# Kernel tuning notes

Hardware: AMD Instinct MI355X
Metric: run time of the kernel (lower is better)

The kernel has to match this reference:

```python
import jax, jax.numpy as jnp
import numpy as np

N = 100000        # nodes
E = 3200000       # edges (avg degree 32)
B = 64            # graphs in the batch
IN_DIM = 128
HEADS = 4
C1 = 8            # conv1 out_channels per head
C2 = 4            # conv2 out_channels per head
OUT_DIM = 10
EPS = 1e-16       # PyG softmax denominator eps


def _lin(key, fan_in, fan_out):
    return jax.random.normal(key, (fan_in, fan_out), jnp.float32) / np.sqrt(fan_in)


def setup_inputs() -> dict:
    key = jax.random.key(0)
    ks = jax.random.split(key, 16)
    x = jax.random.normal(ks[0], (N, IN_DIM), jnp.float32)
    edge_index = jax.random.randint(ks[1], (2, E), 0, N)
    batch = jnp.sort(jax.random.randint(ks[2], (N,), 0, B))
    d1 = HEADS * C1  # 32
    d2 = HEADS * C2  # 16
    inp = {
        "x": x, "edge_index": edge_index, "batch": batch,
        # conv1 (TransformerConv in=128 -> heads*8 = 32)
        "Wq1": _lin(ks[3], IN_DIM, d1), "bq1": jnp.zeros((d1,), jnp.float32),
        "Wk1": _lin(ks[4], IN_DIM, d1), "bk1": jnp.zeros((d1,), jnp.float32),
        "Wv1": _lin(ks[5], IN_DIM, d1), "bv1": jnp.zeros((d1,), jnp.float32),
        "Ws1": _lin(ks[6], IN_DIM, d1), "bs1": jnp.zeros((d1,), jnp.float32),
        # conv2 (in=32 -> heads*4 = 16)
        "Wq2": _lin(ks[7], d1, d2), "bq2": jnp.zeros((d2,), jnp.float32),
        "Wk2": _lin(ks[8], d1, d2), "bk2": jnp.zeros((d2,), jnp.float32),
        "Wv2": _lin(ks[9], d1, d2), "bv2": jnp.zeros((d2,), jnp.float32),
        "Ws2": _lin(ks[10], d1, d2), "bs2": jnp.zeros((d2,), jnp.float32),
        # fc (16 -> 10)
        "Wfc": _lin(ks[11], d2, OUT_DIM), "bfc": jnp.zeros((OUT_DIM,), jnp.float32),
    }
    return inp


def transformer_conv(x, src, dst, Wq, bq, Wk, bk, Wv, bv, Ws, bs, heads):
    n = x.shape[0]
    hc = Wq.shape[1]
    c = hc // heads
    q = (x @ Wq + bq).reshape(n, heads, c)
    k = (x @ Wk + bk).reshape(n, heads, c)
    v = (x @ Wv + bv).reshape(n, heads, c)
    # edge-wise attention logits: query at dst, key at src -> [E, H]
    alpha = jnp.einsum('ehc,ehc->eh', q[dst], k[src]) / np.sqrt(c).astype(np.float32)
    # segment softmax over incoming edges of each dst node
    amax = jax.ops.segment_max(alpha, dst, num_segments=n)           # [N,H]
    ea = jnp.exp(alpha - amax[dst])
    denom = jax.ops.segment_sum(ea, dst, num_segments=n)             # [N,H]
    w = ea / (denom[dst] + EPS)                                      # [E,H]
    msg = v[src] * w[:, :, None]                                     # [E,H,C]
    out = jax.ops.segment_sum(msg, dst, num_segments=n).reshape(n, hc)
    return out + x @ Ws + bs  # root/skip connection


def reference(x, edge_index, batch,
              Wq1, bq1, Wk1, bk1, Wv1, bv1, Ws1, bs1,
              Wq2, bq2, Wk2, bk2, Wv2, bv2, Ws2, bs2,
              Wfc, bfc):
    src, dst = edge_index[0], edge_index[1]
    h = transformer_conv(x, src, dst, Wq1, bq1, Wk1, bk1, Wv1, bv1, Ws1, bs1, HEADS)
    h = jax.nn.relu(h)
    h = transformer_conv(h, src, dst, Wq2, bq2, Wk2, bk2, Wv2, bv2, Ws2, bs2, HEADS)
    h = jax.nn.relu(h)
    # global mean pool per graph
    sums = jax.ops.segment_sum(h, batch, num_segments=B)             # [B,16]
    cnt = jax.ops.segment_sum(jnp.ones((h.shape[0],), h.dtype), batch, num_segments=B)
    pooled = sums / jnp.maximum(cnt, 1.0)[:, None]
    return pooled @ Wfc + bfc                                        # [B,OUT_DIM]
```

## Files before the change

### kernel.cpp

```cpp
#include <hip/hip_runtime.h>

#define HEADS 4
#define EPS 1e-16f
#define NR 256
#define EPB 2048

typedef float floatx2 __attribute__((ext_vector_type(2)));
typedef short bf16x8 __attribute__((ext_vector_type(8)));
typedef float f32x4 __attribute__((ext_vector_type(4)));

__device__ inline unsigned short f2bf(float f) {
    union { float f; unsigned u; } v; v.f = f;
    unsigned r = v.u + 0x7FFFu + ((v.u >> 16) & 1u);
    return (unsigned short)(r >> 16);
}
__device__ inline unsigned char f2fp8(float f) {
    return (unsigned char)(__builtin_amdgcn_cvt_pk_fp8_f32(f, 0.f, 0u, false) & 0xFF);
}

__device__ inline int rangeOf(int dst, int rdiv, float rinv) {
    int q = (int)((float)dst * rinv);
    if (q > NR - 1) q = NR - 1;
    if ((long long)q * rdiv > dst) --q;
    else if ((long long)(q + 1) * rdiv <= dst) ++q;
    return q;
}

__global__ __launch_bounds__(256) void scatter_count(
    const int* __restrict__ ei, int E, int rdiv, float rinv,
    int* __restrict__ pcnt)
{
    __shared__ int cnt[NR];
    int b = blockIdx.x, t = threadIdx.x;
    int b0 = b * EPB;
    int nloc = min(EPB, E - b0);
    cnt[t] = 0;
    __syncthreads();
    #pragma unroll
    for (int u = 0; u < 8; ++u) {
        int li = u * 256 + t;
        if (li < nloc)
            atomicAdd(&cnt[rangeOf(ei[E + b0 + li], rdiv, rinv)], 1);
    }
    __syncthreads();
    pcnt[(size_t)b * NR + t] = cnt[t];
}

__global__ __launch_bounds__(256) void qprefix(
    int* __restrict__ pcnt, int nb, int* __restrict__ qtot)
{
    __shared__ int part[256];
    int q = blockIdx.x, t = threadIdx.x;
    int per = (nb + 255) >> 8;
    int lo = t * per, hi = min(lo + per, nb);
    int s = 0;
    for (int b = lo; b < hi; ++b) s += pcnt[(size_t)b * NR + q];
    part[t] = s;
    __syncthreads();
    for (int off = 1; off < 256; off <<= 1) {
        int a = (t >= off) ? part[t - off] : 0;
        __syncthreads();
        part[t] += a;
        __syncthreads();
    }
    if (t == 255) qtot[q] = part[255];
    int pre = (t == 0) ? 0 : part[t - 1];
    for (int b = lo; b < hi; ++b) {
        int c = pcnt[(size_t)b * NR + q];
        pcnt[(size_t)b * NR + q] = pre;
        pre += c;
    }
}

__global__ void qscan(const int* __restrict__ qtot, int* __restrict__ rstart)
{
    __shared__ int tmp[NR];
    int t = threadIdx.x;
    tmp[t] = qtot[t];
    __syncthreads();
    for (int off = 1; off < NR; off <<= 1) {
        int a = (t >= off) ? tmp[t - off] : 0;
        __syncthreads();
        tmp[t] += a;
        __syncthreads();
    }
    rstart[t] = (t == 0) ? 0 : tmp[t - 1];
    if (t == NR - 1) rstart[NR] = tmp[NR - 1];
}

__global__ __launch_bounds__(256) void scatter_place(
    const int* __restrict__ ei, int E, int rdiv, float rinv,
    const int* __restrict__ pcnt, const int* __restrict__ rstart,
    int* __restrict__ rsrc, int* __restrict__ rdst)
{
    __shared__ int2 lrec[EPB];
    __shared__ unsigned char lq[EPB];
    __shared__ int cnt[NR], base[NR], scn[NR];
    int b = blockIdx.x, t = threadIdx.x;
    int b0 = b * EPB;
    int nloc = min(EPB, E - b0);
    cnt[t] = 0;
    __syncthreads();
    int myq[8], myoff[8];
    int2 myrec[8];
    #pragma unroll
    for (int u = 0; u < 8; ++u) {
        int li = u * 256 + t;
        if (li < nloc) {
            int e = b0 + li;
            int sv = ei[e], dv = ei[E + e];
            int q = rangeOf(dv, rdiv, rinv);
            myq[u] = q;
            myrec[u] = make_int2(sv, dv);
            myoff[u] = atomicAdd(&cnt[q], 1);
        } else myq[u] = -1;
    }
    __syncthreads();
    scn[t] = cnt[t];
    __syncthreads();
    for (int off = 1; off < 256; off <<= 1) {
        int a = (t >= off) ? scn[t - off] : 0;
        __syncthreads();
        scn[t] += a;
        __syncthreads();
    }
    base[t] = (t == 0) ? 0 : scn[t - 1];
    __syncthreads();
    #pragma unroll
    for (int u = 0; u < 8; ++u) {
        if (myq[u] >= 0) {
            int slot = base[myq[u]] + myoff[u];
            lrec[slot] = myrec[u];
            lq[slot] = (unsigned char)myq[u];
        }
    }
    __syncthreads();
    #pragma unroll
    for (int u = 0; u < 8; ++u) {
        int s2 = u * 256 + t;
        if (s2 < nloc) {
            int q = lq[s2];
            int g = rstart[q] + pcnt[(size_t)b * NR + q] + (s2 - base[q]);
            int2 r = lrec[s2];
            rsrc[g] = r.x;
            rdst[g] = r.y;
        }
    }
}

__global__ __launch_bounds__(256) void deg_range_place(
    const int* __restrict__ rsrc, const int* __restrict__ rdst,
    const int* __restrict__ rstart,
    int* __restrict__ deg, int* __restrict__ row_ptr, int* __restrict__ phd,
    int* __restrict__ col, int n, int rdiv, int E)
{
    __shared__ int h[512];
    __shared__ int cur[512];
    __shared__ int psum[256];
    __shared__ int hd[256];
    int q = blockIdx.x, t = threadIdx.x;
    int lo = q * rdiv, hi = min(lo + rdiv, n);
    int nn = hi - lo;
    if (nn <= 0) {
        phd[q * 256 + t] = 0;
        if (t == 0 && q == NR - 1) row_ptr[n] = E;
        return;
    }
    h[t] = 0; h[t + 256] = 0; hd[t] = 0;
    __syncthreads();
    int rlo = rstart[q], rhi = rstart[q + 1];
    for (int i = rlo + t; i < rhi; i += 256)
        atomicAdd(&h[rdst[i] - lo], 1);
    __syncthreads();
    int s0 = h[2 * t], s1 = h[2 * t + 1];
    psum[t] = s0 + s1;
    __syncthreads();
    for (int off = 1; off < 256; off <<= 1) {
        int a = (t >= off) ? psum[t - off] : 0;
        __syncthreads();
        psum[t] += a;
        __syncthreads();
    }
    int base = rlo + ((t == 0) ? 0 : psum[t - 1]);
    cur[2 * t] = base;
    cur[2 * t + 1] = base + s0;
    if (2 * t < nn) {
        row_ptr[lo + 2 * t] = base;
        deg[lo + 2 * t] = s0;
        atomicAdd(&hd[min(s0, 255)], 1);
    }
    if (2 * t + 1 < nn) {
        row_ptr[lo + 2 * t + 1] = base + s0;
        deg[lo + 2 * t + 1] = s1;
        atomicAdd(&hd[min(s1, 255)], 1);
    }
    if (t == 0 && q == NR - 1) row_ptr[n] = E;
    __syncthreads();
    phd[q * 256 + t] = hd[t];
    for (int i = rlo + t; i < rhi; i += 256) {
        int pos = atomicAdd(&cur[rdst[i] - lo], 1);
        col[pos] = rsrc[i];
    }
}

__global__ __launch_bounds__(256) void dsort_scanA(
    int* __restrict__ phd, int* __restrict__ tot)
{
    __shared__ int tmp[256];
    int bin = blockIdx.x, t = threadIdx.x;
    int v = phd[t * 256 + bin];
    tmp[t] = v;
    __syncthreads();
    for (int off = 1; off < 256; off <<= 1) {
        int a = (t >= off) ? tmp[t - off] : 0;
        __syncthreads();
        tmp[t] += a;
        __syncthreads();
    }
    phd[t * 256 + bin] = tmp[t] - v;
    if (t == 255) tot[bin] = tmp[255];
}

__global__ void dsort_scanB(int* __restrict__ tot)
{
    __shared__ int tmp[256];
    int t = threadIdx.x;
    int v = tot[t];
    tmp[t] = v;
    __syncthreads();
    for (int off = 1; off < 256; off <<= 1) {
        int a = (t >= off) ? tmp[t - off] : 0;
        __syncthreads();
        tmp[t] += a;
        __syncthreads();
    }
    tot[t] = tmp[t] - v;
}

__global__ __launch_bounds__(256) void dsort_place(
    const int* __restrict__ phd, const int* __restrict__ tot,
    const int* __restrict__ deg, int* __restrict__ order, int n, int rdiv)
{
    __shared__ int lcur[256];
    int q = blockIdx.x, t = threadIdx.x;
    lcur[t] = phd[q * 256 + t] + tot[t];
    __syncthreads();
    int lo = q * rdiv, hi = min(lo + rdiv, n);
    for (int i = lo + t; i < hi; i += 256) {
        int pos = atomicAdd(&lcur[min(deg[i], 255)], 1);
        order[pos] = i;
    }
}

__global__ __launch_bounds__(256) void pack_w1(
    const float* __restrict__ Wq, const float* __restrict__ Wk,
    const float* __restrict__ Wv, const float* __restrict__ Ws,
    unsigned short* __restrict__ wp)
{
    int tid = blockIdx.x * 256 + threadIdx.x;
    int s = tid >> 9, c = (tid >> 6) & 7, l = tid & 63;
    int gcol = c * 16 + (l & 15);
    int sub = gcol >> 5, j = gcol & 31;
    const float* W = (sub == 0) ? Wq : (sub == 1) ? Wk : (sub == 2) ? Wv : Ws;
    int k0 = s * 32 + ((l >> 4) << 3);
    unsigned short v[8];
    #pragma unroll
    for (int jj = 0; jj < 8; ++jj) v[jj] = f2bf(W[(size_t)(k0 + jj) * 32 + j]);
    uint4 o;
    o.x = v[0] | ((unsigned)v[1] << 16);
    o.y = v[2] | ((unsigned)v[3] << 16);
    o.z = v[4] | ((unsigned)v[5] << 16);
    o.w = v[6] | ((unsigned)v[7] << 16);
    *(uint4*)(wp + (size_t)tid * 8) = o;
}

__global__ void pack_w2(
    const float* __restrict__ Wq, const float* __restrict__ Wk,
    const float* __restrict__ Wv, const float* __restrict__ Ws,
    unsigned short* __restrict__ wp)
{
    int tid = threadIdx.x;
    int c = tid >> 6, l = tid & 63;
    int gcol = c * 16 + (l & 15);
    int sub = gcol >> 4, j = gcol & 15;
    const float* W = (sub == 0) ? Wq : (sub == 1) ? Wk : (sub == 2) ? Wv : Ws;
    int k0 = (l >> 4) << 3;
    unsigned short v[8];
    #pragma unroll
    for (int jj = 0; jj < 8; ++jj) v[jj] = f2bf(W[(size_t)(k0 + jj) * 16 + j]);
    uint4 o;
    o.x = v[0] | ((unsigned)v[1] << 16);
    o.y = v[2] | ((unsigned)v[3] << 16);
    o.z = v[4] | ((unsigned)v[5] << 16);
    o.w = v[6] | ((unsigned)v[7] << 16);
    *(uint4*)(wp + (size_t)tid * 8) = o;
}

__global__ __launch_bounds__(256) void proj1_mfma(
    const float* __restrict__ x, const unsigned short* __restrict__ wp,
    const float* __restrict__ bq, const float* __restrict__ bk,
    const float* __restrict__ bv, const float* __restrict__ bs,
    float* __restrict__ qs1, unsigned char* __restrict__ kv1, int n)
{
    int w = threadIdx.x >> 6, l = threadIdx.x & 63;
    int row0 = blockIdx.x * 64 + w * 16;
    if (row0 >= n) return;
    int arow = row0 + (l & 15);
    f32x4 c0 = {0,0,0,0}, c1 = {0,0,0,0}, c2 = {0,0,0,0}, c3 = {0,0,0,0};
    f32x4 c4 = {0,0,0,0}, c5 = {0,0,0,0}, c6 = {0,0,0,0}, c7 = {0,0,0,0};
    const uint4* wp4 = (const uint4*)wp;
    #pragma unroll
    for (int s = 0; s < 4; ++s) {
        union { uint4 u; bf16x8 b; } av;
        if (arow < n) {
            const float* xp = x + (size_t)arow * 128 + s * 32 + ((l >> 4) << 3);
            float4 x0 = *(const float4*)xp;
            float4 x1 = *(const float4*)(xp + 4);
            av.u.x = f2bf(x0.x) | ((unsigned)f2bf(x0.y) << 16);
            av.u.y = f2bf(x0.z) | ((unsigned)f2bf(x0.w) << 16);
            av.u.z = f2bf(x1.x) | ((unsigned)f2bf(x1.y) << 16);
            av.u.w = f2bf(x1.z) | ((unsigned)f2bf(x1.w) << 16);
        } else {
            av.u = make_uint4(0, 0, 0, 0);
        }
        const uint4* base = wp4 + (size_t)(s * 8) * 64 + l;
        union { uint4 u; bf16x8 b; } bc;
        bc.u = base[0 * 64]; c0 = __builtin_amdgcn_mfma_f32_16x16x32_bf16(av.b, bc.b, c0, 0, 0, 0);
        bc.u = base[1 * 64]; c1 = __builtin_amdgcn_mfma_f32_16x16x32_bf16(av.b, bc.b, c1, 0, 0, 0);
        bc.u = base[2 * 64]; c2 = __builtin_amdgcn_mfma_f32_16x16x32_bf16(av.b, bc.b, c2, 0, 0, 0);
        bc.u = base[3 * 64]; c3 = __builtin_amdgcn_mfma_f32_16x16x32_bf16(av.b, bc.b, c3, 0, 0, 0);
        bc.u = base[4 * 64]; c4 = __builtin_amdgcn_mfma_f32_16x16x32_bf16(av.b, bc.b, c4, 0, 0, 0);
        bc.u = base[5 * 64]; c5 = __builtin_amdgcn_mfma_f32_16x16x32_bf16(av.b, bc.b, c5, 0, 0, 0);
        bc.u = base[6 * 64]; c6 = __builtin_amdgcn_mfma_f32_16x16x32_bf16(av.b, bc.b, c6, 0, 0, 0);
        bc.u = base[7 * 64]; c7 = __builtin_amdgcn_mfma_f32_16x16x32_bf16(av.b, bc.b, c7, 0, 0, 0);
    }
    int rbase = row0 + ((l >> 4) << 2);
    int lc = l & 15;
    int pkA = ((lc >> 3) << 4) + (lc & 7);
    int pkB = ((2 + (lc >> 3)) << 4) + (lc & 7);
    int pvA = pkA + 8;
    int pvB = pkB + 8;
    float bq0 = bq[lc], bq1 = bq[16 + lc];
    float bk0 = bk[lc], bk1 = bk[16 + lc];
    float bv0 = bv[lc], bv1 = bv[16 + lc];
    float bs0 = bs[lc], bs1 = bs[16 + lc];
    #pragma unroll
    for (int r = 0; r < 4; ++r) {
        int row = rbase + r;
        if (row < n) {
            float* q = qs1 + (size_t)row * 64;
            unsigned char* kvp = kv1 + (size_t)row * 64;
            q[lc]      = c0[r] + bq0;
            q[16 + lc] = c1[r] + bq1;
            q[32 + lc] = c6[r] + bs0;
            q[48 + lc] = c7[r] + bs1;
            kvp[pkA] = f2fp8(c2[r] + bk0);
            kvp[pkB] = f2fp8(c3[r] + bk1);
            kvp[pvA] = f2fp8(c4[r] + bv0);
            kvp[pvB] = f2fp8(c5[r] + bv1);
        }
    }
}

__global__ __launch_bounds__(256) void proj2_mfma(
    const float* __restrict__ h1, const unsigned short* __restrict__ wp,
    const float* __restrict__ bq, const float* __restrict__ bk,
    const float* __restrict__ bv, const float* __restrict__ bs,
    float* __restrict__ qs2, unsigned char* __restrict__ kv2, int n)
{
    int w = threadIdx.x >> 6, l = threadIdx.x & 63;
    int row0 = blockIdx.x * 64 + w * 16;
    if (row0 >= n) return;
    int arow = row0 + (l & 15);
    f32x4 c0 = {0,0,0,0}, c1 = {0,0,0,0}, c2 = {0,0,0,0}, c3 = {0,0,0,0};
    union { uint4 u; bf16x8 b; } av;
    if (arow < n) {
        const float* xp = h1 + (size_t)arow * 32 + ((l >> 4) << 3);
        float4 x0 = *(const float4*)xp;
        float4 x1 = *(const float4*)(xp + 4);
        av.u.x = f2bf(x0.x) | ((unsigned)f2bf(x0.y) << 16);
        av.u.y = f2bf(x0.z) | ((unsigned)f2bf(x0.w) << 16);
        av.u.z = f2bf(x1.x) | ((unsigned)f2bf(x1.y) << 16);
        av.u.w = f2bf(x1.z) | ((unsigned)f2bf(x1.w) << 16);
    } else {
        av.u = make_uint4(0, 0, 0, 0);
    }
    const uint4* base = (const uint4*)wp + l;
    union { uint4 u; bf16x8 b; } bc;
    bc.u = base[0];   c0 = __builtin_amdgcn_mfma_f32_16x16x32_bf16(av.b, bc.b, c0, 0, 0, 0);
    bc.u = base[64];  c1 = __builtin_amdgcn_mfma_f32_16x16x32_bf16(av.b, bc.b, c1, 0, 0, 0);
    bc.u = base[128]; c2 = __builtin_amdgcn_mfma_f32_16x16x32_bf16(av.b, bc.b, c2, 0, 0, 0);
    bc.u = base[192]; c3 = __builtin_amdgcn_mfma_f32_16x16x32_bf16(av.b, bc.b, c3, 0, 0, 0);
    int rbase = row0 + ((l >> 4) << 2);
    int lc = l & 15;
    int pk = ((lc >> 2) << 3) + (lc & 3);
    int pv = pk + 4;
    float bq0 = bq[lc], bk0 = bk[lc], bv0 = bv[lc], bs0 = bs[lc];
    #pragma unroll
    for (int r = 0; r < 4; ++r) {
        int row = rbase + r;
        if (row < n) {
            float* q = qs2 + (size_t)row * 32;
            unsigned char* kvp = kv2 + (size_t)row * 32;
            q[lc]      = c0[r] + bq0;
            q[16 + lc] = c3[r] + bs0;
            kvp[pk] = f2fp8(c1[r] + bk0);
            kvp[pv] = f2fp8(c2[r] + bv0);
        }
    }
}

__global__ __launch_bounds__(256) void gather_conv1(
    const int* __restrict__ row_ptr, const int* __restrict__ order,
    const int* __restrict__ col, const float* __restrict__ qs1,
    const unsigned char* __restrict__ kv1, float* __restrict__ h1, int n)
{
    int tid = blockIdx.x * 256 + threadIdx.x;
    if (tid >= n * HEADS) return;
    int node = order[tid >> 2], h = tid & 3;
    const float4* qp = (const float4*)(qs1 + (size_t)node * 64 + h * 8);
    float4 q0 = qp[0], q1 = qp[1];
    int start = row_ptr[node], d = row_ptr[node + 1] - start;
    float m = -INFINITY, s = 0.f;
    float a0x=0,a0y=0,a0z=0,a0w=0,a1x=0,a1y=0,a1z=0,a1w=0;
    if (d > 0) {
        int dm1 = d - 1;
        uint4 kv = *(const uint4*)(kv1 + (size_t)col[start] * 64 + h * 16);
        int c1 = col[start + min(1, dm1)];
        for (int i = 0; i < d; ++i) {
            int c2 = col[start + min(i + 2, dm1)];
            uint4 kvn = *(const uint4*)(kv1 + (size_t)c1 * 64 + h * 16);
            floatx2 k01 = __builtin_amdgcn_cvt_pk_f32_fp8(kv.x, false);
            floatx2 k23 = __builtin_amdgcn_cvt_pk_f32_fp8(kv.x, true);
            floatx2 k45 = __builtin_amdgcn_cvt_pk_f32_fp8(kv.y, false);
            floatx2 k67 = __builtin_amdgcn_cvt_pk_f32_fp8(kv.y, true);
            float a = (q0.x*k01.x + q0.y*k01.y + q0.z*k23.x + q0.w*k23.y
                     + q1.x*k45.x + q1.y*k45.y + q1.z*k67.x + q1.w*k67.y)
                    * 0.35355339059327373f;
            float mn = fmaxf(m, a);
            float corr = __expf(m - mn);
            float ea = __expf(a - mn);
            s = s * corr + ea;
            floatx2 v01 = __builtin_amdgcn_cvt_pk_f32_fp8(kv.z, false);
            floatx2 v23 = __builtin_amdgcn_cvt_pk_f32_fp8(kv.z, true);
            floatx2 v45 = __builtin_amdgcn_cvt_pk_f32_fp8(kv.w, false);
            floatx2 v67 = __builtin_amdgcn_cvt_pk_f32_fp8(kv.w, true);
            a0x = a0x*corr + ea*v01.x; a0y = a0y*corr + ea*v01.y;
            a0z = a0z*corr + ea*v23.x; a0w = a0w*corr + ea*v23.y;
            a1x = a1x*corr + ea*v45.x; a1y = a1y*corr + ea*v45.y;
            a1z = a1z*corr + ea*v67.x; a1w = a1w*corr + ea*v67.y;
            m = mn;
            kv = kvn; c1 = c2;
        }
    }
    float inv = 1.f / (s + EPS);
    const float* sk = qs1 + (size_t)node * 64 + 32 + h * 8;
    float4 o0, o1;
    o0.x = fmaxf(a0x*inv + sk[0], 0.f); o0.y = fmaxf(a0y*inv + sk[1], 0.f);
    o0.z = fmaxf(a0z*inv + sk[2], 0.f); o0.w = fmaxf(a0w*inv + sk[3], 0.f);
    o1.x = fmaxf(a1x*inv + sk[4], 0.f); o1.y = fmaxf(a1y*inv + sk[5], 0.f);
    o1.z = fmaxf(a1z*inv + sk[6], 0.f); o1.w = fmaxf(a1w*inv + sk[7], 0.f);
    float4* op = (float4*)(h1 + (size_t)node * 32 + h * 8);
    op[0] = o0; op[1] = o1;
}

__global__ __launch_bounds__(256) void gather_conv2(
    const int* __restrict__ row_ptr, const int* __restrict__ order,
    const int* __restrict__ col, const float* __restrict__ qs2,
    const unsigned char* __restrict__ kv2, float* __restrict__ h2, int n)
{
    int tid = blockIdx.x * 256 + threadIdx.x;
    if (tid >= n * HEADS) return;
    int node = order[tid >> 2], h = tid & 3;
    float4 q = *(const float4*)(qs2 + (size_t)node * 32 + h * 4);
    int start = row_ptr[node], d = row_ptr[node + 1] - start;
    float m = -INFINITY, s = 0.f;
    float ax=0, ay=0, az=0, aw=0;
    if (d > 0) {
        int dm1 = d - 1;
        uint2 kv = *(const uint2*)(kv2 + (size_t)col[start] * 32 + h * 8);
        int c1 = col[start + min(1, dm1)];
        for (int i = 0; i < d; ++i) {
            int c2 = col[start + min(i + 2, dm1)];
            uint2 kvn = *(const uint2*)(kv2 + (size_t)c1 * 32 + h * 8);
            floatx2 k01 = __builtin_amdgcn_cvt_pk_f32_fp8(kv.x, false);
            floatx2 k23 = __builtin_amdgcn_cvt_pk_f32_fp8(kv.x, true);
            float a = (q.x*k01.x + q.y*k01.y + q.z*k23.x + q.w*k23.y) * 0.5f;
            float mn = fmaxf(m, a);
            float corr = __expf(m - mn);
            float ea = __expf(a - mn);
            s = s * corr + ea;
            floatx2 v01 = __builtin_amdgcn_cvt_pk_f32_fp8(kv.y, false);
            floatx2 v23 = __builtin_amdgcn_cvt_pk_f32_fp8(kv.y, true);
            ax = ax*corr + ea*v01.x; ay = ay*corr + ea*v01.y;
            az = az*corr + ea*v23.x; aw = aw*corr + ea*v23.y;
            m = mn;
            kv = kvn; c1 = c2;
        }
    }
    float inv = 1.f / (s + EPS);
    const float* sk = qs2 + (size_t)node * 32 + 16 + h * 4;
    float4 o;
    o.x = fmaxf(ax*inv + sk[0], 0.f);
    o.y = fmaxf(ay*inv + sk[1], 0.f);
    o.z = fmaxf(az*inv + sk[2], 0.f);
    o.w = fmaxf(aw*inv + sk[3], 0.f);
    *(float4*)(h2 + (size_t)node * 16 + h * 4) = o;
}

__global__ __launch_bounds__(256) void pool_kernel(
    const float* __restrict__ h2, const int* __restrict__ batch,
    float* __restrict__ pooled, float* __restrict__ cnt, int n)
{
    __shared__ float acc[16];
    __shared__ int bShared;
    __shared__ int uniform;
    int node0 = blockIdx.x * 16;
    int t = threadIdx.x;
    int node = node0 + (t >> 4), j = t & 15;
    if (t == 0) {
        int bFirst = batch[node0];
        int bLast = batch[min(node0 + 15, n - 1)];
        bShared = bFirst;
        uniform = (bFirst == bLast);
    }
    if (t < 16) acc[t] = 0.f;
    __syncthreads();
    bool active = node < n;
    float val = active ? h2[(size_t)node * 16 + j] : 0.f;
    if (uniform) {
        if (active) atomicAdd(&acc[j], val);
        __syncthreads();
        int nlocal = min(16, n - node0);
        if (t < 16) atomicAdd(pooled + bShared * 16 + t, acc[t]);
        if (t == 0) atomicAdd(cnt + bShared, (float)nlocal);
    } else {
        if (active) {
            int b = batch[node];
            atomicAdd(pooled + b * 16 + j, val);
            if (j == 0) atomicAdd(cnt + b, 1.f);
        }
    }
}

__global__ void fc_kernel(
    const float* __restrict__ pooled, const float* __restrict__ cnt,
    const float* __restrict__ Wfc, const float* __restrict__ bfc,
    float* __restrict__ out)
{
    int t = threadIdx.x;
    if (t < 64 * 10) {
        int b = t / 10, o = t % 10;
        float c = fmaxf(cnt[b], 1.0f);
        float acc = bfc[o];
        #pragma unroll
        for (int k = 0; k < 16; ++k)
            acc += (pooled[b * 16 + k] / c) * Wfc[k * 10 + o];
        out[t] = acc;
    }
}

extern "C" void kernel_launch(void* const* d_in, const int* in_sizes, int n_in,
                              void* d_out, int out_size, void* d_ws, size_t ws_size,
                              hipStream_t stream) {
    const float* x     = (const float*)d_in[0];
    const int*   ei    = (const int*)d_in[1];
    const int*   batch = (const int*)d_in[2];
    const float* Wq1 = (const float*)d_in[3],  *bq1 = (const float*)d_in[4];
    const float* Wk1 = (const float*)d_in[5],  *bk1 = (const float*)d_in[6];
    const float* Wv1 = (const float*)d_in[7],  *bv1 = (const float*)d_in[8];
    const float* Ws1 = (const float*)d_in[9],  *bs1 = (const float*)d_in[10];
    const float* Wq2 = (const float*)d_in[11], *bq2 = (const float*)d_in[12];
    const float* Wk2 = (const float*)d_in[13], *bk2 = (const float*)d_in[14];
    const float* Wv2 = (const float*)d_in[15], *bv2 = (const float*)d_in[16];
    const float* Ws2 = (const float*)d_in[17], *bs2 = (const float*)d_in[18];
    const float* Wfc = (const float*)d_in[19], *bfc = (const float*)d_in[20];

    int N = in_sizes[0] / 128;
    int E = in_sizes[1] / 2;
    int rdiv = (N + NR - 1) / NR;
    float rinv = 1.0f / (float)rdiv;
    int NB = (E + EPB - 1) / EPB;

    float* ws = (float*)d_ws;
    float* qs1    = ws;
    float* h1     = qs1 + (size_t)N * 64;
    float* h2     = h1 + (size_t)N * 32;
    float* qs2    = h2 + (size_t)N * 16;
    float* pooled = qs2 + (size_t)N * 32;
    float* cnt    = pooled + 1024;
    unsigned char* kv1 = (unsigned char*)(cnt + 64);
    unsigned char* kv2 = kv1 + (size_t)N * 64;
    int* deg     = (int*)(kv2 + (size_t)N * 32);
    int* row_ptr = deg + N;
    int* rstart  = row_ptr + N + 1;
    int* qtot    = rstart + NR + 1;
    int* col     = qtot + NR;
    int* order   = col + E;
    int* pcnt    = order + N;
    int* phd     = pcnt + (size_t)NB * NR;
    unsigned short* wp1 = (unsigned short*)(phd + (size_t)NR * 256);
    unsigned short* wp2 = wp1 + 16384;
    int* rsrc = (int*)h1;
    int* rdst = (int*)h2;

    hipMemsetAsync(pooled, 0, (1024 + 64) * sizeof(float), stream);

    int ngrid = (N * HEADS + 255) / 256;
    int mtiles = (N + 63) / 64;

    pack_w1<<<8, 256, 0, stream>>>(Wq1, Wk1, Wv1, Ws1, wp1);
    pack_w2<<<1, 256, 0, stream>>>(Wq2, Wk2, Wv2, Ws2, wp2);

    scatter_count<<<NB, 256, 0, stream>>>(ei, E, rdiv, rinv, pcnt);
    qprefix<<<NR, 256, 0, stream>>>(pcnt, NB, qtot);
    qscan<<<1, NR, 0, stream>>>(qtot, rstart);
    scatter_place<<<NB, 256, 0, stream>>>(ei, E, rdiv, rinv, pcnt, rstart, rsrc, rdst);
    deg_range_place<<<NR, 256, 0, stream>>>(rsrc, rdst, rstart, deg, row_ptr, phd, col, N, rdiv, E);
    dsort_scanA<<<NR, 256, 0, stream>>>(phd, qtot);
    dsort_scanB<<<1, 256, 0, stream>>>(qtot);
    dsort_place<<<NR, 256, 0, stream>>>(phd, qtot, deg, order, N, rdiv);

    proj1_mfma<<<mtiles, 256, 0, stream>>>(x, wp1, bq1, bk1, bv1, bs1, qs1, kv1, N);
    gather_conv1<<<ngrid, 256, 0, stream>>>(row_ptr, order, col, qs1, kv1, h1, N);

    proj2_mfma<<<mtiles, 256, 0, stream>>>(h1, wp2, bq2, bk2, bv2, bs2, qs2, kv2, N);
    gather_conv2<<<ngrid, 256, 0, stream>>>(row_ptr, order, col, qs2, kv2, h2, N);

    pool_kernel<<<(N + 15) / 16, 256, 0, stream>>>(h2, batch, pooled, cnt, N);
    fc_kernel<<<1, 640, 0, stream>>>(pooled, cnt, Wfc, bfc, (float*)d_out);
}
```

Measured before the change: 312.1 us.

## Store K/V head-major and assign one head per gather block

Projection kernels now write fp8 K/V in a head-major layout ([head][node][16 or 8 bytes]) instead of node-major. The gather kernels map each block to a single head, so every thread gathers from a compact per-head array. This aims to shrink each head's working set and improve cache-line use per head. The cost is that the four heads of a node are no longer read by adjacent lanes, so row_ptr, col and q loads are repeated across blocks and a shared 64B line is split into separate accesses.

New measurement: 705.7 us. 2.26x slower.

```diff
diff --git a/kernel.cpp b/kernel.cpp
--- a/kernel.cpp
+++ b/kernel.cpp
@@ -336,10 +336,8 @@
     }
     int rbase = row0 + ((l >> 4) << 2);
     int lc = l & 15;
-    int pkA = ((lc >> 3) << 4) + (lc & 7);
-    int pkB = ((2 + (lc >> 3)) << 4) + (lc & 7);
-    int pvA = pkA + 8;
-    int pvB = pkB + 8;
+    int hA = lc >> 3, eA = lc & 7;
+    int hB = 2 + (lc >> 3);
     float bq0 = bq[lc], bq1 = bq[16 + lc];
     float bk0 = bk[lc], bk1 = bk[16 + lc];
     float bv0 = bv[lc], bv1 = bv[16 + lc];
@@ -349,15 +347,14 @@
         int row = rbase + r;
         if (row < n) {
             float* q = qs1 + (size_t)row * 64;
-            unsigned char* kvp = kv1 + (size_t)row * 64;
             q[lc]      = c0[r] + bq0;
             q[16 + lc] = c1[r] + bq1;
             q[32 + lc] = c6[r] + bs0;
             q[48 + lc] = c7[r] + bs1;
-            kvp[pkA] = f2fp8(c2[r] + bk0);
-            kvp[pkB] = f2fp8(c3[r] + bk1);
-            kvp[pvA] = f2fp8(c4[r] + bv0);
-            kvp[pvB] = f2fp8(c5[r] + bv1);
+            kv1[((size_t)hA * n + row) * 16 + eA]     = f2fp8(c2[r] + bk0);
+            kv1[((size_t)hB * n + row) * 16 + eA]     = f2fp8(c3[r] + bk1);
+            kv1[((size_t)hA * n + row) * 16 + 8 + eA] = f2fp8(c4[r] + bv0);
+            kv1[((size_t)hB * n + row) * 16 + 8 + eA] = f2fp8(c5[r] + bv1);
         }
     }
 }
@@ -393,19 +390,17 @@
     bc.u = base[192]; c3 = __builtin_amdgcn_mfma_f32_16x16x32_bf16(av.b, bc.b, c3, 0, 0, 0);
     int rbase = row0 + ((l >> 4) << 2);
     int lc = l & 15;
-    int pk = ((lc >> 2) << 3) + (lc & 3);
-    int pv = pk + 4;
+    int hh = lc >> 2, ee = lc & 3;
     float bq0 = bq[lc], bk0 = bk[lc], bv0 = bv[lc], bs0 = bs[lc];
     #pragma unroll
     for (int r = 0; r < 4; ++r) {
         int row = rbase + r;
         if (row < n) {
             float* q = qs2 + (size_t)row * 32;
-            unsigned char* kvp = kv2 + (size_t)row * 32;
             q[lc]      = c0[r] + bq0;
             q[16 + lc] = c3[r] + bs0;
-            kvp[pk] = f2fp8(c1[r] + bk0);
-            kvp[pv] = f2fp8(c2[r] + bv0);
+            kv2[((size_t)hh * n + row) * 8 + ee]     = f2fp8(c1[r] + bk0);
+            kv2[((size_t)hh * n + row) * 8 + 4 + ee] = f2fp8(c2[r] + bv0);
         }
     }
 }
@@ -415,9 +410,11 @@
     const int* __restrict__ col, const float* __restrict__ qs1,
     const unsigned char* __restrict__ kv1, float* __restrict__ h1, int n)
 {
-    int tid = blockIdx.x * 256 + threadIdx.x;
-    if (tid >= n * HEADS) return;
-    int node = order[tid >> 2], h = tid & 3;
+    int h = blockIdx.x & 3;
+    int idx = (blockIdx.x >> 2) * 256 + threadIdx.x;
+    if (idx >= n) return;
+    int node = order[idx];
+    const unsigned char* kvh = kv1 + (size_t)h * n * 16;
     const float4* qp = (const float4*)(qs1 + (size_t)node * 64 + h * 8);
     float4 q0 = qp[0], q1 = qp[1];
     int start = row_ptr[node], d = row_ptr[node + 1] - start;
@@ -425,11 +422,11 @@
     float a0x=0,a0y=0,a0z=0,a0w=0,a1x=0,a1y=0,a1z=0,a1w=0;
     if (d > 0) {
         int dm1 = d - 1;
-        uint4 kv = *(const uint4*)(kv1 + (size_t)col[start] * 64 + h * 16);
+        uint4 kv = *(const uint4*)(kvh + (size_t)col[start] * 16);
         int c1 = col[start + min(1, dm1)];
         for (int i = 0; i < d; ++i) {
             int c2 = col[start + min(i + 2, dm1)];
-            uint4 kvn = *(const uint4*)(kv1 + (size_t)c1 * 64 + h * 16);
+            uint4 kvn = *(const uint4*)(kvh + (size_t)c1 * 16);
             floatx2 k01 = __builtin_amdgcn_cvt_pk_f32_fp8(kv.x, false);
             floatx2 k23 = __builtin_amdgcn_cvt_pk_f32_fp8(kv.x, true);
             floatx2 k45 = __builtin_amdgcn_cvt_pk_f32_fp8(kv.y, false);
@@ -469,20 +466,22 @@
     const int* __restrict__ col, const float* __restrict__ qs2,
     const unsigned char* __restrict__ kv2, float* __restrict__ h2, int n)
 {
-    int tid = blockIdx.x * 256 + threadIdx.x;
-    if (tid >= n * HEADS) return;
-    int node = order[tid >> 2], h = tid & 3;
+    int h = blockIdx.x & 3;
+    int idx = (blockIdx.x >> 2) * 256 + threadIdx.x;
+    if (idx >= n) return;
+    int node = order[idx];
+    const unsigned char* kvh = kv2 + (size_t)h * n * 8;
     float4 q = *(const float4*)(qs2 + (size_t)node * 32 + h * 4);
     int start = row_ptr[node], d = row_ptr[node + 1] - start;
     float m = -INFINITY, s = 0.f;
     float ax=0, ay=0, az=0, aw=0;
     if (d > 0) {
         int dm1 = d - 1;
-        uint2 kv = *(const uint2*)(kv2 + (size_t)col[start] * 32 + h * 8);
+        uint2 kv = *(const uint2*)(kvh + (size_t)col[start] * 8);
         int c1 = col[start + min(1, dm1)];
         for (int i = 0; i < d; ++i) {
             int c2 = col[start + min(i + 2, dm1)];
-            uint2 kvn = *(const uint2*)(kv2 + (size_t)c1 * 32 + h * 8);
+            uint2 kvn = *(const uint2*)(kvh + (size_t)c1 * 8);
             floatx2 k01 = __builtin_amdgcn_cvt_pk_f32_fp8(kv.x, false);
             floatx2 k23 = __builtin_amdgcn_cvt_pk_f32_fp8(kv.x, true);
             float a = (q.x*k01.x + q.y*k01.y + q.z*k23.x + q.w*k23.y) * 0.5f;
@@ -606,7 +605,7 @@
 
     hipMemsetAsync(pooled, 0, (1024 + 64) * sizeof(float), stream);
 
-    int ngrid = (N * HEADS + 255) / 256;
+    int ggrid = 4 * ((N + 255) / 256);
     int mtiles = (N + 63) / 64;
 
     pack_w1<<<8, 256, 0, stream>>>(Wq1, Wk1, Wv1, Ws1, wp1);
@@ -622,10 +621,10 @@
     dsort_place<<<NR, 256, 0, stream>>>(phd, qtot, deg, order, N, rdiv);
 
     proj1_mfma<<<mtiles, 256, 0, stream>>>(x, wp1, bq1, bk1, bv1, bs1, qs1, kv1, N);
-    gather_conv1<<<ngrid, 256, 0, stream>>>(row_ptr, order, col, qs1, kv1, h1, N);
+    gather_conv1<<<ggrid, 256, 0, stream>>>(row_ptr, order, col, qs1, kv1, h1, N);
 
     proj2_mfma<<<mtiles, 256, 0, stream>>>(h1, wp2, bq2, bk2, bv2, bs2, qs2, kv2, N);
-    gather_conv2<<<ngrid, 256, 0, stream>>>(row_ptr, order, col, qs2, kv2, h2, N);
+    gather_conv2<<<ggrid, 256, 0, stream>>>(row_ptr, order, col, qs2, kv2, h2, N);
 
     pool_kernel<<<(N + 15) / 16, 256, 0, stream>>>(h2, batch, pooled, cnt, N);
     fc_kernel<<<1, 640, 0, stream>>>(pooled, cnt, Wfc, bfc, (float*)d_out);
```
